# Optimization experiments

Hardware: AMD Instinct MI355X
Metric: run time of the kernel (lower is better)

Reference implementation:

```python
import jax, jax.numpy as jnp
import numpy as np

L, K, H = 8000, 48, 128
SCALE = 30.0
LN_EPS = 1e-5


def _gelu(x):
    return jax.nn.gelu(x, approximate=False)


def _ln(x, s, o):
    mu = x.mean(-1, keepdims=True)
    var = ((x - mu) ** 2).mean(-1, keepdims=True)
    return (x - mu) * jax.lax.rsqrt(var + LN_EPS) * s + o


def setup_inputs() -> dict:
    key = jax.random.key(0)
    ks = jax.random.split(key, 24)

    def w(k, fan_in, fan_out):
        return (jax.random.normal(k, (fan_in, fan_out), jnp.float32) / np.sqrt(fan_in)).astype(jnp.float32)

    inp = {
        "h_V": jax.random.normal(ks[0], (L, H), jnp.float32),
        "h_E": jax.random.normal(ks[1], (L, K, H), jnp.float32),
        "E_idx": jax.random.randint(ks[2], (L, K), 0, L, jnp.int32),
        "mask_V": jnp.ones((L,), jnp.float32),
        "mask_attend": jnp.ones((L, K), jnp.float32),
        # node-message MLP (W1 consumes [h_V, h_E, gathered h_V] = 3H)
        "W1_w": w(ks[3], 3 * H, H), "W1_b": jnp.zeros((H,), jnp.float32),
        "W2_w": w(ks[4], H, H),     "W2_b": jnp.zeros((H,), jnp.float32),
        "W3_w": w(ks[5], H, H),     "W3_b": jnp.zeros((H,), jnp.float32),
        # edge-update MLP
        "W11_w": w(ks[6], 3 * H, H), "W11_b": jnp.zeros((H,), jnp.float32),
        "W12_w": w(ks[7], H, H),     "W12_b": jnp.zeros((H,), jnp.float32),
        "W13_w": w(ks[8], H, H),     "W13_b": jnp.zeros((H,), jnp.float32),
        # position-wise FFN (H -> 4H -> H)
        "Wi_w": w(ks[9], H, 4 * H),  "Wi_b": jnp.zeros((4 * H,), jnp.float32),
        "Wo_w": w(ks[10], 4 * H, H), "Wo_b": jnp.zeros((H,), jnp.float32),
        # layer norms
        "n1_s": jnp.ones((H,), jnp.float32), "n1_o": jnp.zeros((H,), jnp.float32),
        "n2_s": jnp.ones((H,), jnp.float32), "n2_o": jnp.zeros((H,), jnp.float32),
        "n3_s": jnp.ones((H,), jnp.float32), "n3_o": jnp.zeros((H,), jnp.float32),
    }
    return inp


def _forward(h_V, h_E, mask_V, mask_attend, E_idx,
             W1_w, W1_b, W2_w, W2_b, W3_w, W3_b,
             W11_w, W11_b, W12_w, W12_b, W13_w, W13_b,
             Wi_w, Wi_b, Wo_w, Wo_b,
             n1_s, n1_o, n2_s, n2_o, n3_s, n3_o):
    # --- node update ---
    nb = h_V[E_idx]                                          # (L,K,H) gather_nodes
    hv_exp = jnp.broadcast_to(h_V[:, None, :], nb.shape)     # (L,K,H)
    h_EV = jnp.concatenate([hv_exp, h_E, nb], -1)            # (L,K,3H)
    m = _gelu(h_EV @ W1_w + W1_b)
    m = _gelu(m @ W2_w + W2_b)
    m = m @ W3_w + W3_b                                      # (L,K,H)
    m = mask_attend[..., None] * m
    dh = m.sum(-2) / SCALE                                   # (L,H)
    hV = _ln(h_V + dh, n1_s, n1_o)                           # dropout = identity (eval)
    d = _gelu(hV @ Wi_w + Wi_b) @ Wo_w + Wo_b                # FFN
    hV = _ln(hV + d, n2_s, n2_o)
    hV = mask_V[:, None] * hV
    # --- edge update ---
    nb2 = hV[E_idx]                                          # (L,K,H)
    hv_exp2 = jnp.broadcast_to(hV[:, None, :], nb2.shape)
    h_EV2 = jnp.concatenate([hv_exp2, h_E, nb2], -1)         # (L,K,3H)
    m2 = _gelu(h_EV2 @ W11_w + W11_b)
    m2 = _gelu(m2 @ W12_w + W12_b)
    m2 = m2 @ W13_w + W13_b
    hE = _ln(h_E + m2, n3_s, n3_o)
    return hV, hE


def reference(h_V, h_E, E_idx, mask_V, mask_attend,
              W1_w, W1_b, W2_w, W2_b, W3_w, W3_b,
              W11_w, W11_b, W12_w, W12_b, W13_w, W13_b,
              Wi_w, Wi_b, Wo_w, Wo_b,
              n1_s, n1_o, n2_s, n2_o, n3_s, n3_o):
    return _forward(h_V, h_E, mask_V, mask_attend, E_idx,
                    W1_w, W1_b, W2_w, W2_b, W3_w, W3_b,
                    W11_w, W11_b, W12_w, W12_b, W13_w, W13_b,
                    Wi_w, Wi_b, Wo_w, Wo_b,
                    n1_s, n1_o, n2_s, n2_o, n3_s, n3_o)
```

## Files before the change

### kernel.cpp

```cpp
#include <hip/hip_runtime.h>
#include <cstddef>
#include <cstdint>
#include <cmath>

#define LDIM 8000
#define KNB  48
#define HDIM 128

typedef short  bf16x8 __attribute__((ext_vector_type(8)));
typedef float  f32x4  __attribute__((ext_vector_type(4)));

__device__ __forceinline__ float gelu_f(float x) {
    return 0.5f * x * (1.0f + erff(x * 0.70710678118654752440f));
}
__device__ __forceinline__ unsigned short bf16_rne(float x) {
    unsigned u = __float_as_uint(x);
    return (unsigned short)((u + 0x7FFFu + ((u >> 16) & 1u)) >> 16);
}
__device__ __forceinline__ float bf16_f(unsigned short h) {
    return __uint_as_float((unsigned)h << 16);
}
__device__ __forceinline__ void split2(float x, short& h, short& l) {
    unsigned short hb = bf16_rne(x);
    h = (short)hb;
    l = (short)bf16_rne(x - bf16_f(hb));
}
__device__ __forceinline__ void mm3(f32x4& c, bf16x8 ah, bf16x8 al, bf16x8 bh, bf16x8 bl) {
    c = __builtin_amdgcn_mfma_f32_16x16x32_bf16(ah, bh, c, 0, 0, 0);
    c = __builtin_amdgcn_mfma_f32_16x16x32_bf16(ah, bl, c, 0, 0, 0);
    c = __builtin_amdgcn_mfma_f32_16x16x32_bf16(al, bh, c, 0, 0, 0);
}

__global__ void wsplit_kernel(const float* __restrict__ W, short* __restrict__ dst, int K) {
    int t = blockIdx.x * 256 + threadIdx.x;
    if (t >= K * 128) return;
    int k = t >> 7, n = t & 127;
    float x = W[t];
    short h, l; split2(x, h, l);
    dst[(size_t)n * K + k]         = h;
    dst[(size_t)(128 + n) * K + k] = l;
}

template<bool EDGE>
__global__ __launch_bounds__(256, 2)
void msg_mfma_kernel(const float* __restrict__ hv_src,
                     const float* __restrict__ hEin,
                     const int*   __restrict__ Eidx,
                     const float* __restrict__ mask_att,
                     const short* __restrict__ WaT,
                     const short* __restrict__ WbT,
                     const short* __restrict__ WcT,
                     const float* __restrict__ ba,
                     const float* __restrict__ bb,
                     const float* __restrict__ bc,
                     const float* __restrict__ ln_s,
                     const float* __restrict__ ln_o,
                     float* __restrict__ outp)
{
    __shared__ union {
        short xc[2][96][40];
        short cp[2][96][136];
        float xb[96 * 132];
    } sm;
    __shared__ float mask_s[96];

    const int bid  = blockIdx.x;
    const int n0   = bid * 2;
    const int tid  = threadIdx.x;
    const int w    = tid >> 6;
    const int lane = tid & 63;
    const int lr   = lane & 15;
    const int hgr  = lane >> 4;
    const int colA = w * 32 + lr;
    const int colB = colA + 16;

    if constexpr (!EDGE) {
        if (tid < 96) mask_s[tid] = mask_att[(size_t)n0 * KNB + tid];
    }

    int trow[3], tq[3];
    const float* pV[3]; const float* pE[3]; const float* pN[3];
#pragma unroll
    for (int it = 0; it < 3; it++) {
        const int t   = tid + it * 256;
        const int row = t >> 3, q = t & 7;
        trow[it] = row; tq[it] = q;
        const int node = n0 + (row >= 48 ? 1 : 0);
        pV[it] = hv_src + (size_t)node * HDIM + q * 4;
        pE[it] = hEin + ((size_t)n0 * KNB + row) * HDIM + q * 4;
        const int nb = Eidx[n0 * KNB + row];
        pN[it] = hv_src + (size_t)nb * HDIM + q * 4;
    }

    f32x4 acc[12];

    {
        const float bA = ba[colA], bB = ba[colB];
#pragma unroll
        for (int mt = 0; mt < 6; mt++) {
            acc[mt*2+0] = (f32x4){bA, bA, bA, bA};
            acc[mt*2+1] = (f32x4){bB, bB, bB, bB};
        }
    }
    {
        const short* WaL = WaT + 128 * 384;
#pragma unroll 1
        for (int ks = 0; ks < 12; ks++) {
            const int ko = ks * 32 + hgr * 8;
            bf16x8 bh0 = *(const bf16x8*)(WaT + (size_t)colA * 384 + ko);
            bf16x8 bl0 = *(const bf16x8*)(WaL + (size_t)colA * 384 + ko);
            bf16x8 bh1 = *(const bf16x8*)(WaT + (size_t)colB * 384 + ko);
            bf16x8 bl1 = *(const bf16x8*)(WaL + (size_t)colB * 384 + ko);
            __syncthreads();
            {
                const int seg = ks >> 2, co = (ks & 3) * 32;
#pragma unroll
                for (int it = 0; it < 3; it++) {
                    const float* p = (seg == 0) ? pV[it] : (seg == 1) ? pE[it] : pN[it];
                    const float4 v = *(const float4*)(p + co);
                    short h0,l0,h1,l1,h2,l2,h3,l3;
                    split2(v.x,h0,l0); split2(v.y,h1,l1);
                    split2(v.z,h2,l2); split2(v.w,h3,l3);
                    *(short4*)&sm.xc[0][trow[it]][tq[it]*4] = make_short4(h0,h1,h2,h3);
                    *(short4*)&sm.xc[1][trow[it]][tq[it]*4] = make_short4(l0,l1,l2,l3);
                }
            }
            __syncthreads();
#pragma unroll
            for (int mt = 0; mt < 6; mt++) {
                bf16x8 ah = *(const bf16x8*)&sm.xc[0][mt*16 + lr][hgr*8];
                bf16x8 al = *(const bf16x8*)&sm.xc[1][mt*16 + lr][hgr*8];
                mm3(acc[mt*2+0], ah, al, bh0, bl0);
                mm3(acc[mt*2+1], ah, al, bh1, bl1);
            }
        }
    }
    __syncthreads();
#pragma unroll
    for (int mt = 0; mt < 6; mt++)
#pragma unroll
    for (int nt = 0; nt < 2; nt++) {
        const int col = w*32 + nt*16 + lr;
        const f32x4 a = acc[mt*2+nt];
#pragma unroll
        for (int j = 0; j < 4; j++) {
            const int row = mt*16 + hgr*4 + j;
            short h, l; split2(gelu_f(a[j]), h, l);
            sm.cp[0][row][col] = h;
            sm.cp[1][row][col] = l;
        }
    }
    __syncthreads();

    {
        const short* WbL = WbT + 128 * 128;
        const float bA = bb[colA], bB = bb[colB];
#pragma unroll
        for (int mt = 0; mt < 6; mt++) {
            acc[mt*2+0] = (f32x4){bA, bA, bA, bA};
            acc[mt*2+1] = (f32x4){bB, bB, bB, bB};
        }
#pragma unroll 1
        for (int ks = 0; ks < 4; ks++) {
            const int ko = ks * 32 + hgr * 8;
            bf16x8 bh0 = *(const bf16x8*)(WbT + (size_t)colA * 128 + ko);
            bf16x8 bl0 = *(const bf16x8*)(WbL + (size_t)colA * 128 + ko);
            bf16x8 bh1 = *(const bf16x8*)(WbT + (size_t)colB * 128 + ko);
            bf16x8 bl1 = *(const bf16x8*)(WbL + (size_t)colB * 128 + ko);
#pragma unroll
            for (int mt = 0; mt < 6; mt++) {
                bf16x8 ah = *(const bf16x8*)&sm.cp[0][mt*16 + lr][ko];
                bf16x8 al = *(const bf16x8*)&sm.cp[1][mt*16 + lr][ko];
                mm3(acc[mt*2+0], ah, al, bh0, bl0);
                mm3(acc[mt*2+1], ah, al, bh1, bl1);
            }
        }
        __syncthreads();
#pragma unroll
        for (int mt = 0; mt < 6; mt++)
#pragma unroll
        for (int nt = 0; nt < 2; nt++) {
            const int col = w*32 + nt*16 + lr;
            const f32x4 a = acc[mt*2+nt];
#pragma unroll
            for (int j = 0; j < 4; j++) {
                const int row = mt*16 + hgr*4 + j;
                short h, l; split2(gelu_f(a[j]), h, l);
                sm.cp[0][row][col] = h;
                sm.cp[1][row][col] = l;
            }
        }
        __syncthreads();
    }

    {
        const short* WcL = WcT + 128 * 128;
        const float bA = bc[colA], bB = bc[colB];
#pragma unroll
        for (int mt = 0; mt < 6; mt++) {
            acc[mt*2+0] = (f32x4){bA, bA, bA, bA};
            acc[mt*2+1] = (f32x4){bB, bB, bB, bB};
        }
#pragma unroll 1
        for (int ks = 0; ks < 4; ks++) {
            const int ko = ks * 32 + hgr * 8;
            bf16x8 bh0 = *(const bf16x8*)(WcT + (size_t)colA * 128 + ko);
            bf16x8 bl0 = *(const bf16x8*)(WcL + (size_t)colA * 128 + ko);
            bf16x8 bh1 = *(const bf16x8*)(WcT + (size_t)colB * 128 + ko);
            bf16x8 bl1 = *(const bf16x8*)(WcL + (size_t)colB * 128 + ko);
#pragma unroll
            for (int mt = 0; mt < 6; mt++) {
                bf16x8 ah = *(const bf16x8*)&sm.cp[0][mt*16 + lr][ko];
                bf16x8 al = *(const bf16x8*)&sm.cp[1][mt*16 + lr][ko];
                mm3(acc[mt*2+0], ah, al, bh0, bl0);
                mm3(acc[mt*2+1], ah, al, bh1, bl1);
            }
        }
        __syncthreads();
    }

    if constexpr (!EDGE) {
        float s[4] = {0.f, 0.f, 0.f, 0.f};
#pragma unroll
        for (int mt = 0; mt < 6; mt++) {
            const int nodei = (mt >= 3) ? 1 : 0;
#pragma unroll
            for (int j = 0; j < 4; j++) {
                const float m = mask_s[mt*16 + hgr*4 + j];
                s[nodei*2+0] = fmaf(m, acc[mt*2+0][j], s[nodei*2+0]);
                s[nodei*2+1] = fmaf(m, acc[mt*2+1][j], s[nodei*2+1]);
            }
        }
#pragma unroll
        for (int i = 0; i < 4; i++) {
            s[i] += __shfl_xor(s[i], 16, 64);
            s[i] += __shfl_xor(s[i], 32, 64);
        }
        if (lane < 16) {
            outp[(size_t)n0 * HDIM + colA]       = s[0] * (1.0f / 30.0f);
            outp[(size_t)n0 * HDIM + colB]       = s[1] * (1.0f / 30.0f);
            outp[(size_t)(n0+1) * HDIM + colA]   = s[2] * (1.0f / 30.0f);
            outp[(size_t)(n0+1) * HDIM + colB]   = s[3] * (1.0f / 30.0f);
        }
    } else {
#pragma unroll
        for (int mt = 0; mt < 6; mt++)
#pragma unroll
        for (int nt = 0; nt < 2; nt++) {
            const int col = w*32 + nt*16 + lr;
            const f32x4 a = acc[mt*2+nt];
#pragma unroll
            for (int j = 0; j < 4; j++) {
                const int row = mt*16 + hgr*4 + j;
                const float he = hEin[((size_t)n0 * KNB + row) * HDIM + col];
                sm.xb[row * 132 + col] = a[j] + he;
            }
        }
        __syncthreads();
        for (int r = w; r < 96; r += 4) {
            const float x0 = sm.xb[r * 132 + lane];
            const float x1 = sm.xb[r * 132 + 64 + lane];
            float su = x0 + x1;
#pragma unroll
            for (int off = 32; off; off >>= 1) su += __shfl_xor(su, off, 64);
            const float mu = su * (1.0f / 128.0f);
            const float d0 = x0 - mu, d1 = x1 - mu;
            float v = d0 * d0 + d1 * d1;
#pragma unroll
            for (int off = 32; off; off >>= 1) v += __shfl_xor(v, off, 64);
            const float rs = rsqrtf(v * (1.0f / 128.0f) + 1e-5f);
            const size_t base = ((size_t)n0 * KNB + r) * HDIM;
            outp[base + lane]      = d0 * rs * ln_s[lane]      + ln_o[lane];
            outp[base + 64 + lane] = d1 * rs * ln_s[64 + lane] + ln_o[64 + lane];
        }
    }
}

template<int RT, int KDIM>
__device__ __forceinline__ void gemm_block(
    const float* __restrict__ A, const int lda,
    const float* __restrict__ Wg, const int wstride,
    float* __restrict__ Wst,
    float acc[RT][4], const int rg, const int jg, const int tid)
{
#pragma unroll 1
    for (int ci = 0; ci < KDIM / 32; ci++) {
        __syncthreads();
#pragma unroll
        for (int e = tid; e < 1024; e += 256) {
            const int i  = e >> 5;
            const int j4 = (e & 31) << 2;
            *(float4*)(Wst + i * 128 + j4) =
                *(const float4*)(Wg + (size_t)(ci * 32 + i) * wstride + j4);
        }
        __syncthreads();
#pragma unroll
        for (int ii = 0; ii < 32; ii += 4) {
            float4 xr[RT];
#pragma unroll
            for (int rr = 0; rr < RT; rr++)
                xr[rr] = *(const float4*)(A + (rg * RT + rr) * lda + ci * 32 + ii);
#pragma unroll
            for (int q = 0; q < 4; q++) {
                const float4 wv = *(const float4*)(Wst + (ii + q) * 128 + (jg << 2));
#pragma unroll
                for (int rr = 0; rr < RT; rr++) {
                    const float x = (q == 0) ? xr[rr].x : (q == 1) ? xr[rr].y
                                  : (q == 2) ? xr[rr].z : xr[rr].w;
                    acc[rr][0] = fmaf(x, wv.x, acc[rr][0]);
                    acc[rr][1] = fmaf(x, wv.y, acc[rr][1]);
                    acc[rr][2] = fmaf(x, wv.z, acc[rr][2]);
                    acc[rr][3] = fmaf(x, wv.w, acc[rr][3]);
                }
            }
        }
    }
}

template<int NPART>
__global__ __launch_bounds__(256, 2)
void node_update_kernel(const float* __restrict__ hV,
                        const float* __restrict__ dhp,
                        const float* __restrict__ maskV,
                        const float* __restrict__ Wi, const float* __restrict__ bi,
                        const float* __restrict__ Wo, const float* __restrict__ bo,
                        const float* __restrict__ n1s, const float* __restrict__ n1o,
                        const float* __restrict__ n2s, const float* __restrict__ n2o,
                        float* __restrict__ outp)
{
    __shared__ float hv1[32 * 128];
    __shared__ float Wst[32 * 128];
    __shared__ float tb[32 * 128];

    const int l0  = blockIdx.x * 32;
    const int tid = threadIdx.x;
    const int w = tid >> 6, ln = tid & 63;

    for (int r = w; r < 32; r += 4) {
        const int l = l0 + r;
        const size_t b = (size_t)l * 128;
        float x0 = hV[b + ln], x1 = hV[b + 64 + ln];
#pragma unroll
        for (int p = 0; p < NPART; p++) {
            x0 += dhp[((size_t)l * NPART + p) * 128 + ln];
            x1 += dhp[((size_t)l * NPART + p) * 128 + 64 + ln];
        }
        float s = x0 + x1;
#pragma unroll
        for (int off = 32; off; off >>= 1) s += __shfl_xor(s, off, 64);
        const float mu = s * (1.0f / 128.0f);
        const float d0 = x0 - mu, d1 = x1 - mu;
        float v = d0 * d0 + d1 * d1;
#pragma unroll
        for (int off = 32; off; off >>= 1) v += __shfl_xor(v, off, 64);
        const float rs = rsqrtf(v * (1.0f / 128.0f) + 1e-5f);
        hv1[r * 128 + ln]      = d0 * rs * n1s[ln]      + n1o[ln];
        hv1[r * 128 + 64 + ln] = d1 * rs * n1s[64 + ln] + n1o[64 + ln];
    }

    const int rg = tid >> 5, jg = tid & 31;
    float dacc[4][4];
#pragma unroll
    for (int rr = 0; rr < 4; rr++)
#pragma unroll
        for (int q = 0; q < 4; q++) dacc[rr][q] = bo[(jg << 2) + q];

#pragma unroll 1
    for (int hc = 0; hc < 4; hc++) {
        float tacc[4][4];
#pragma unroll
        for (int rr = 0; rr < 4; rr++)
#pragma unroll
            for (int q = 0; q < 4; q++) tacc[rr][q] = bi[hc * 128 + (jg << 2) + q];
        gemm_block<4, 128>(hv1, 128, Wi + hc * 128, 512, Wst, tacc, rg, jg, tid);
        __syncthreads();
#pragma unroll
        for (int rr = 0; rr < 4; rr++)
#pragma unroll
            for (int q = 0; q < 4; q++)
                tb[(rg * 4 + rr) * 128 + (jg << 2) + q] = gelu_f(tacc[rr][q]);
        gemm_block<4, 128>(tb, 128, Wo + (size_t)hc * 128 * 128, 128, Wst, dacc, rg, jg, tid);
    }
    __syncthreads();
#pragma unroll
    for (int rr = 0; rr < 4; rr++)
#pragma unroll
        for (int q = 0; q < 4; q++)
            tb[(rg * 4 + rr) * 128 + (jg << 2) + q] = dacc[rr][q];
    __syncthreads();

    for (int r = w; r < 32; r += 4) {
        const int l = l0 + r;
        const float x0 = hv1[r * 128 + ln]      + tb[r * 128 + ln];
        const float x1 = hv1[r * 128 + 64 + ln] + tb[r * 128 + 64 + ln];
        float s = x0 + x1;
#pragma unroll
        for (int off = 32; off; off >>= 1) s += __shfl_xor(s, off, 64);
        const float mu = s * (1.0f / 128.0f);
        const float d0 = x0 - mu, d1 = x1 - mu;
        float v = d0 * d0 + d1 * d1;
#pragma unroll
        for (int off = 32; off; off >>= 1) v += __shfl_xor(v, off, 64);
        const float rs = rsqrtf(v * (1.0f / 128.0f) + 1e-5f);
        const float mv = maskV[l];
        outp[(size_t)l * 128 + ln]      = mv * (d0 * rs * n2s[ln]      + n2o[ln]);
        outp[(size_t)l * 128 + 64 + ln] = mv * (d1 * rs * n2s[64 + ln] + n2o[64 + ln]);
    }
}

template<bool EDGE>
__global__ __launch_bounds__(256, 2)
void msg_kernel(const float* __restrict__ hv_src,
                const float* __restrict__ hEin,
                const int*   __restrict__ Eidx,
                const float* __restrict__ mask_att,
                const float* __restrict__ Wa, const float* __restrict__ ba,
                const float* __restrict__ Wb, const float* __restrict__ bb,
                const float* __restrict__ Wc3, const float* __restrict__ bc,
                const float* __restrict__ ln_s, const float* __restrict__ ln_o,
                float* __restrict__ outp)
{
    __shared__ float xs[24 * 384];
    __shared__ float Wst[32 * 128];
    __shared__ float Cb[24 * 128];

    const int bid = blockIdx.x;
    const int l   = bid >> 1;
    const int k0  = (bid & 1) * 24;
    const int tid = threadIdx.x;

#pragma unroll
    for (int e = tid; e < 24 * 32; e += 256) {
        const int r  = e >> 5;
        const int c4 = (e & 31) << 2;
        const int k  = k0 + r;
        const int nidx = Eidx[l * KNB + k];
        const float4 hv4 = *(const float4*)(hv_src + (size_t)l * HDIM + c4);
        const float4 he4 = *(const float4*)(hEin + ((size_t)l * KNB + k) * HDIM + c4);
        const float4 nb4 = *(const float4*)(hv_src + (size_t)nidx * HDIM + c4);
        *(float4*)(xs + r * 384 +       c4) = hv4;
        *(float4*)(xs + r * 384 + 128 + c4) = he4;
        *(float4*)(xs + r * 384 + 256 + c4) = nb4;
    }

    const int rg = tid >> 5;
    const int jg = tid & 31;
    float acc[3][4];

#pragma unroll
    for (int rr = 0; rr < 3; rr++)
#pragma unroll
        for (int q = 0; q < 4; q++) acc[rr][q] = ba[(jg << 2) + q];
    gemm_block<3, 384>(xs, 384, Wa, 128, Wst, acc, rg, jg, tid);
    __syncthreads();
#pragma unroll
    for (int rr = 0; rr < 3; rr++)
#pragma unroll
        for (int q = 0; q < 4; q++)
            Cb[(rg * 3 + rr) * 128 + (jg << 2) + q] = gelu_f(acc[rr][q]);

#pragma unroll
    for (int rr = 0; rr < 3; rr++)
#pragma unroll
        for (int q = 0; q < 4; q++) acc[rr][q] = bb[(jg << 2) + q];
    gemm_block<3, 128>(Cb, 128, Wb, 128, Wst, acc, rg, jg, tid);
    __syncthreads();
#pragma unroll
    for (int rr = 0; rr < 3; rr++)
#pragma unroll
        for (int q = 0; q < 4; q++)
            Cb[(rg * 3 + rr) * 128 + (jg << 2) + q] = gelu_f(acc[rr][q]);

#pragma unroll
    for (int rr = 0; rr < 3; rr++)
#pragma unroll
        for (int q = 0; q < 4; q++) acc[rr][q] = bc[(jg << 2) + q];
    gemm_block<3, 128>(Cb, 128, Wc3, 128, Wst, acc, rg, jg, tid);
    __syncthreads();

    if constexpr (!EDGE) {
        float psum[4] = {0.f, 0.f, 0.f, 0.f};
#pragma unroll
        for (int rr = 0; rr < 3; rr++) {
            const int k = k0 + rg * 3 + rr;
            const float mval = mask_att[l * KNB + k];
#pragma unroll
            for (int q = 0; q < 4; q++) psum[q] = fmaf(mval, acc[rr][q], psum[q]);
        }
#pragma unroll
        for (int q = 0; q < 4; q++) Cb[rg * 128 + (jg << 2) + q] = psum[q];
        __syncthreads();
        if (tid < 128) {
            float s = 0.f;
#pragma unroll
            for (int g = 0; g < 8; g++) s += Cb[g * 128 + tid];
            outp[(size_t)bid * 128 + tid] = s * (1.0f / 30.0f);
        }
    } else {
#pragma unroll
        for (int rr = 0; rr < 3; rr++)
#pragma unroll
            for (int q = 0; q < 4; q++)
                Cb[(rg * 3 + rr) * 128 + (jg << 2) + q] = acc[rr][q];
        __syncthreads();
        const int w = tid >> 6, ln = tid & 63;
        for (int r = w; r < 24; r += 4) {
            const float x0 = Cb[r * 128 + ln]      + xs[r * 384 + 128 + ln];
            const float x1 = Cb[r * 128 + 64 + ln] + xs[r * 384 + 192 + ln];
            float s = x0 + x1;
#pragma unroll
            for (int off = 32; off; off >>= 1) s += __shfl_xor(s, off, 64);
            const float mu = s * (1.0f / 128.0f);
            const float d0 = x0 - mu, d1 = x1 - mu;
            float v = d0 * d0 + d1 * d1;
#pragma unroll
            for (int off = 32; off; off >>= 1) v += __shfl_xor(v, off, 64);
            const float rs = rsqrtf(v * (1.0f / 128.0f) + 1e-5f);
            const size_t base = ((size_t)(l * KNB + k0 + r)) * 128;
            outp[base + ln]      = d0 * rs * ln_s[ln]      + ln_o[ln];
            outp[base + 64 + ln] = d1 * rs * ln_s[64 + ln] + ln_o[64 + ln];
        }
    }
}

extern "C" void kernel_launch(void* const* d_in, const int* in_sizes, int n_in,
                              void* d_out, int out_size, void* d_ws, size_t ws_size,
                              hipStream_t stream) {
    const float* hV      = (const float*)d_in[0];
    const float* hE      = (const float*)d_in[1];
    const int*   Eidx    = (const int*)  d_in[2];
    const float* maskV   = (const float*)d_in[3];
    const float* maskAtt = (const float*)d_in[4];
    const float* W1  = (const float*)d_in[5];  const float* b1  = (const float*)d_in[6];
    const float* W2  = (const float*)d_in[7];  const float* b2  = (const float*)d_in[8];
    const float* W3  = (const float*)d_in[9];  const float* b3  = (const float*)d_in[10];
    const float* W11 = (const float*)d_in[11]; const float* b11 = (const float*)d_in[12];
    const float* W12 = (const float*)d_in[13]; const float* b12 = (const float*)d_in[14];
    const float* W13 = (const float*)d_in[15]; const float* b13 = (const float*)d_in[16];
    const float* Wi  = (const float*)d_in[17]; const float* bi  = (const float*)d_in[18];
    const float* Wo  = (const float*)d_in[19]; const float* bo  = (const float*)d_in[20];
    const float* n1s = (const float*)d_in[21]; const float* n1o = (const float*)d_in[22];
    const float* n2s = (const float*)d_in[23]; const float* n2o = (const float*)d_in[24];
    const float* n3s = (const float*)d_in[25]; const float* n3o = (const float*)d_in[26];

    float* outF  = (float*)d_out;
    float* hVout = outF;
    float* hEout = outF + (size_t)LDIM * HDIM;

    const size_t O_W1T  = 0;
    const size_t O_W2T  = 196608;
    const size_t O_W3T  = 262144;
    const size_t O_W11T = 327680;
    const size_t O_W12T = 524288;
    const size_t O_W13T = 589824;
    const size_t O_DH   = 655360;
    const size_t WS_NEED = O_DH + (size_t)LDIM * HDIM * sizeof(float);

    if (ws_size >= WS_NEED) {
        char* wsb = (char*)d_ws;
        short* W1T  = (short*)(wsb + O_W1T);
        short* W2T  = (short*)(wsb + O_W2T);
        short* W3T  = (short*)(wsb + O_W3T);
        short* W11T = (short*)(wsb + O_W11T);
        short* W12T = (short*)(wsb + O_W12T);
        short* W13T = (short*)(wsb + O_W13T);
        float* dh   = (float*)(wsb + O_DH);

        wsplit_kernel<<<192, 256, 0, stream>>>(W1,  W1T,  384);
        wsplit_kernel<<< 64, 256, 0, stream>>>(W2,  W2T,  128);
        wsplit_kernel<<< 64, 256, 0, stream>>>(W3,  W3T,  128);
        wsplit_kernel<<<192, 256, 0, stream>>>(W11, W11T, 384);
        wsplit_kernel<<< 64, 256, 0, stream>>>(W12, W12T, 128);
        wsplit_kernel<<< 64, 256, 0, stream>>>(W13, W13T, 128);

        msg_mfma_kernel<false><<<LDIM / 2, 256, 0, stream>>>(
            hV, hE, Eidx, maskAtt, W1T, W2T, W3T, b1, b2, b3, nullptr, nullptr, dh);

        node_update_kernel<1><<<LDIM / 32, 256, 0, stream>>>(
            hV, dh, maskV, Wi, bi, Wo, bo, n1s, n1o, n2s, n2o, hVout);

        msg_mfma_kernel<true><<<LDIM / 2, 256, 0, stream>>>(
            hVout, hE, Eidx, nullptr, W11T, W12T, W13T, b11, b12, b13, n3s, n3o, hEout);
    } else {
        const size_t dh_bytes = (size_t)LDIM * 2 * HDIM * sizeof(float);
        float* dhp = (ws_size >= dh_bytes) ? (float*)d_ws : hEout;

        msg_kernel<false><<<LDIM * 2, 256, 0, stream>>>(
            hV, hE, Eidx, maskAtt, W1, b1, W2, b2, W3, b3, nullptr, nullptr, dhp);

        node_update_kernel<2><<<LDIM / 32, 256, 0, stream>>>(
            hV, dhp, maskV, Wi, bi, Wo, bo, n1s, n1o, n2s, n2o, hVout);

        msg_kernel<true><<<LDIM * 2, 256, 0, stream>>>(
            hVout, hE, Eidx, nullptr, W11, b11, W12, b12, W13, b13, n3s, n3o, hEout);
    }
}
```

Before: 1.299 ms.

## Presplit node features to bf16 hi/lo, double-buffer GEMM staging, swizzle LDS rows

Adds a kernel that splits the node-feature matrix into bf16 hi/lo planes once, so the message kernel gathers pre-split halves instead of converting gathered fp32 values per tile. The first GEMM's input staging is double-buffered in shared memory with register prefetch of the next tile and its weights, which removes one barrier per k-step. The 128-wide GEMMs also prefetch weights, and a row permutation is applied when storing activations to cut LDS bank conflicts. The node-update kernel now uses 16-node blocks for more parallelism. The cost is two extra split passes and extra workspace memory.

```diff
diff --git a/kernel.cpp b/kernel.cpp
--- a/kernel.cpp
+++ b/kernel.cpp
@@ -35,18 +35,25 @@
     int t = blockIdx.x * 256 + threadIdx.x;
     if (t >= K * 128) return;
     int k = t >> 7, n = t & 127;
-    float x = W[t];
-    short h, l; split2(x, h, l);
+    short h, l; split2(W[t], h, l);
     dst[(size_t)n * K + k]         = h;
     dst[(size_t)(128 + n) * K + k] = l;
 }
 
+__global__ void hvsplit_kernel(const float* __restrict__ src, short* __restrict__ dst) {
+    int t = blockIdx.x * 256 + threadIdx.x;
+    if (t >= LDIM * HDIM) return;
+    short h, l; split2(src[t], h, l);
+    dst[t] = h;
+    dst[LDIM * HDIM + t] = l;
+}
+
 template<bool EDGE>
 __global__ __launch_bounds__(256, 2)
-void msg_mfma_kernel(const float* __restrict__ hv_src,
-                     const float* __restrict__ hEin,
+void msg_mfma_kernel(const float* __restrict__ hEin,
                      const int*   __restrict__ Eidx,
                      const float* __restrict__ mask_att,
+                     const short* __restrict__ hvP,
                      const short* __restrict__ WaT,
                      const short* __restrict__ WbT,
                      const short* __restrict__ WcT,
@@ -58,7 +65,7 @@
                      float* __restrict__ outp)
 {
     __shared__ union {
-        short xc[2][96][40];
+        short xc[2][2][96][40];
         short cp[2][96][136];
         float xb[96 * 132];
     } sm;
@@ -71,153 +78,152 @@
     const int lane = tid & 63;
     const int lr   = lane & 15;
     const int hgr  = lane >> 4;
+    const int plr  = ((lr & 2) << 2) | ((2 * (lr >> 2) + (lr & 1) + 2 * (lr & 2)) & 7);
     const int colA = w * 32 + lr;
     const int colB = colA + 16;
+    const int PL   = LDIM * HDIM;
 
     if constexpr (!EDGE) {
         if (tid < 96) mask_s[tid] = mask_att[(size_t)n0 * KNB + tid];
     }
 
-    int trow[3], tq[3];
-    const float* pV[3]; const float* pE[3]; const float* pN[3];
+    int xoff[3];
+    int hvo[3], nbo[3];
+    const float* pE[3];
 #pragma unroll
     for (int it = 0; it < 3; it++) {
-        const int t   = tid + it * 256;
-        const int row = t >> 3, q = t & 7;
-        trow[it] = row; tq[it] = q;
+        const int t = tid + it * 256, row = t >> 3, q = t & 7;
+        xoff[it] = row * 40 + q * 4;
         const int node = n0 + (row >= 48 ? 1 : 0);
-        pV[it] = hv_src + (size_t)node * HDIM + q * 4;
-        pE[it] = hEin + ((size_t)n0 * KNB + row) * HDIM + q * 4;
-        const int nb = Eidx[n0 * KNB + row];
-        pN[it] = hv_src + (size_t)nb * HDIM + q * 4;
+        hvo[it] = node * HDIM + q * 4;
+        nbo[it] = Eidx[n0 * KNB + row] * HDIM + q * 4;
+        pE[it]  = hEin + ((size_t)n0 * KNB + row) * HDIM + q * 4;
     }
 
     f32x4 acc[12];
 
-    {
-        const float bA = ba[colA], bB = ba[colB];
+    uint4 sr[3];
+    auto LOADR = [&](int ks) {
+#pragma unroll
+        for (int it = 0; it < 3; it++) {
+            const int seg = ks >> 2, co = (ks & 3) * 32;
+            if (seg == 1) {
+                sr[it] = *(const uint4*)(pE[it] + co);
+            } else {
+                const int base = (seg == 0 ? hvo[it] : nbo[it]) + co;
+                const uint2 h = *(const uint2*)(hvP + base);
+                const uint2 l = *(const uint2*)(hvP + PL + base);
+                sr[it] = make_uint4(h.x, h.y, l.x, l.y);
+            }
+        }
+    };
+    auto WRITES = [&](int ks, int b) {
+        short* p0 = &sm.xc[b][0][0][0];
+        short* p1 = &sm.xc[b][1][0][0];
+#pragma unroll
+        for (int it = 0; it < 3; it++) {
+            if ((ks >> 2) == 1) {
+                const float4 v = *(const float4*)&sr[it];
+                short h0,l0,h1,l1,h2,l2,h3,l3;
+                split2(v.x,h0,l0); split2(v.y,h1,l1);
+                split2(v.z,h2,l2); split2(v.w,h3,l3);
+                *(short4*)(p0 + xoff[it]) = make_short4(h0,h1,h2,h3);
+                *(short4*)(p1 + xoff[it]) = make_short4(l0,l1,l2,l3);
+            } else {
+                *(uint2*)(p0 + xoff[it]) = make_uint2(sr[it].x, sr[it].y);
+                *(uint2*)(p1 + xoff[it]) = make_uint2(sr[it].z, sr[it].w);
+            }
+        }
+    };
+    auto BLOAD = [&](const short* Th, int stride, int ks,
+                     bf16x8& b0, bf16x8& b1, bf16x8& b2, bf16x8& b3) {
+        const short* Tl = Th + 128 * stride;
+        const int ko = ks * 32 + hgr * 8;
+        b0 = *(const bf16x8*)(Th + (size_t)colA * stride + ko);
+        b1 = *(const bf16x8*)(Tl + (size_t)colA * stride + ko);
+        b2 = *(const bf16x8*)(Th + (size_t)colB * stride + ko);
+        b3 = *(const bf16x8*)(Tl + (size_t)colB * stride + ko);
+    };
+    auto storeC = [&]() {
+#pragma unroll
+        for (int mt = 0; mt < 6; mt++)
+#pragma unroll
+        for (int nt = 0; nt < 2; nt++) {
+            const int col = w * 32 + nt * 16 + lr;
+            const f32x4 a = acc[mt * 2 + nt];
+#pragma unroll
+            for (int j = 0; j < 4; j++) {
+                const int prw = mt * 16 +
+                    (((j >> 1) << 3) | ((2 * hgr + (j & 1) + 4 * (j >> 1)) & 7));
+                short h, l; split2(gelu_f(a[j]), h, l);
+                sm.cp[0][prw][col] = h;
+                sm.cp[1][prw][col] = l;
+            }
+        }
+    };
+    auto gemmK128 = [&](const short* T, const float* bias) {
+        const float bA = bias[colA], bB = bias[colB];
 #pragma unroll
         for (int mt = 0; mt < 6; mt++) {
             acc[mt*2+0] = (f32x4){bA, bA, bA, bA};
             acc[mt*2+1] = (f32x4){bB, bB, bB, bB};
         }
-    }
+        bf16x8 c0,c1,c2,c3,d0,d1,d2,d3;
+        BLOAD(T, 128, 0, c0,c1,c2,c3);
+#pragma unroll 1
+        for (int ks = 0; ks < 4; ks++) {
+            if (ks < 3) BLOAD(T, 128, ks + 1, d0,d1,d2,d3);
+            const int ko = ks * 32 + hgr * 8;
+#pragma unroll
+            for (int mt = 0; mt < 6; mt++) {
+                bf16x8 ah = *(const bf16x8*)&sm.cp[0][mt*16 + plr][ko];
+                bf16x8 al = *(const bf16x8*)&sm.cp[1][mt*16 + plr][ko];
+                mm3(acc[mt*2+0], ah, al, c0, c1);
+                mm3(acc[mt*2+1], ah, al, c2, c3);
+            }
+            c0=d0; c1=d1; c2=d2; c3=d3;
+        }
+    };
+
     {
-        const short* WaL = WaT + 128 * 384;
-#pragma unroll 1
-        for (int ks = 0; ks < 12; ks++) {
-            const int ko = ks * 32 + hgr * 8;
-            bf16x8 bh0 = *(const bf16x8*)(WaT + (size_t)colA * 384 + ko);
-            bf16x8 bl0 = *(const bf16x8*)(WaL + (size_t)colA * 384 + ko);
-            bf16x8 bh1 = *(const bf16x8*)(WaT + (size_t)colB * 384 + ko);
-            bf16x8 bl1 = *(const bf16x8*)(WaL + (size_t)colB * 384 + ko);
-            __syncthreads();
-            {
-                const int seg = ks >> 2, co = (ks & 3) * 32;
-#pragma unroll
-                for (int it = 0; it < 3; it++) {
-                    const float* p = (seg == 0) ? pV[it] : (seg == 1) ? pE[it] : pN[it];
-                    const float4 v = *(const float4*)(p + co);
-                    short h0,l0,h1,l1,h2,l2,h3,l3;
-                    split2(v.x,h0,l0); split2(v.y,h1,l1);
-                    split2(v.z,h2,l2); split2(v.w,h3,l3);
-                    *(short4*)&sm.xc[0][trow[it]][tq[it]*4] = make_short4(h0,h1,h2,h3);
-                    *(short4*)&sm.xc[1][trow[it]][tq[it]*4] = make_short4(l0,l1,l2,l3);
-                }
-            }
-            __syncthreads();
-#pragma unroll
-            for (int mt = 0; mt < 6; mt++) {
-                bf16x8 ah = *(const bf16x8*)&sm.xc[0][mt*16 + lr][hgr*8];
-                bf16x8 al = *(const bf16x8*)&sm.xc[1][mt*16 + lr][hgr*8];
-                mm3(acc[mt*2+0], ah, al, bh0, bl0);
-                mm3(acc[mt*2+1], ah, al, bh1, bl1);
-            }
-        }
-    }
-    __syncthreads();
-#pragma unroll
-    for (int mt = 0; mt < 6; mt++)
-#pragma unroll
-    for (int nt = 0; nt < 2; nt++) {
-        const int col = w*32 + nt*16 + lr;
-        const f32x4 a = acc[mt*2+nt];
-#pragma unroll
-        for (int j = 0; j < 4; j++) {
-            const int row = mt*16 + hgr*4 + j;
-            short h, l; split2(gelu_f(a[j]), h, l);
-            sm.cp[0][row][col] = h;
-            sm.cp[1][row][col] = l;
-        }
-    }
-    __syncthreads();
-
-    {
-        const short* WbL = WbT + 128 * 128;
-        const float bA = bb[colA], bB = bb[colB];
+        const float bA = ba[colA], bB = ba[colB];
 #pragma unroll
         for (int mt = 0; mt < 6; mt++) {
             acc[mt*2+0] = (f32x4){bA, bA, bA, bA};
             acc[mt*2+1] = (f32x4){bB, bB, bB, bB};
         }
+    }
+    {
+        bf16x8 c0,c1,c2,c3,d0,d1,d2,d3;
+        LOADR(0);
+        BLOAD(WaT, 384, 0, c0,c1,c2,c3);
+        WRITES(0, 0);
+        __syncthreads();
 #pragma unroll 1
-        for (int ks = 0; ks < 4; ks++) {
-            const int ko = ks * 32 + hgr * 8;
-            bf16x8 bh0 = *(const bf16x8*)(WbT + (size_t)colA * 128 + ko);
-            bf16x8 bl0 = *(const bf16x8*)(WbL + (size_t)colA * 128 + ko);
-            bf16x8 bh1 = *(const bf16x8*)(WbT + (size_t)colB * 128 + ko);
-            bf16x8 bl1 = *(const bf16x8*)(WbL + (size_t)colB * 128 + ko);
+        for (int ks = 0; ks < 12; ks++) {
+            if (ks < 11) { LOADR(ks + 1); BLOAD(WaT, 384, ks + 1, d0,d1,d2,d3); }
+            const int b = ks & 1;
 #pragma unroll
             for (int mt = 0; mt < 6; mt++) {
-                bf16x8 ah = *(const bf16x8*)&sm.cp[0][mt*16 + lr][ko];
-                bf16x8 al = *(const bf16x8*)&sm.cp[1][mt*16 + lr][ko];
-                mm3(acc[mt*2+0], ah, al, bh0, bl0);
-                mm3(acc[mt*2+1], ah, al, bh1, bl1);
-            }
-        }
-        __syncthreads();
-#pragma unroll
-        for (int mt = 0; mt < 6; mt++)
-#pragma unroll
-        for (int nt = 0; nt < 2; nt++) {
-            const int col = w*32 + nt*16 + lr;
-            const f32x4 a = acc[mt*2+nt];
-#pragma unroll
-            for (int j = 0; j < 4; j++) {
-                const int row = mt*16 + hgr*4 + j;
-                short h, l; split2(gelu_f(a[j]), h, l);
-                sm.cp[0][row][col] = h;
-                sm.cp[1][row][col] = l;
-            }
-        }
-        __syncthreads();
-    }
-
-    {
-        const short* WcL = WcT + 128 * 128;
-        const float bA = bc[colA], bB = bc[colB];
-#pragma unroll
-        for (int mt = 0; mt < 6; mt++) {
-            acc[mt*2+0] = (f32x4){bA, bA, bA, bA};
-            acc[mt*2+1] = (f32x4){bB, bB, bB, bB};
-        }
-#pragma unroll 1
-        for (int ks = 0; ks < 4; ks++) {
-            const int ko = ks * 32 + hgr * 8;
-            bf16x8 bh0 = *(const bf16x8*)(WcT + (size_t)colA * 128 + ko);
-            bf16x8 bl0 = *(const bf16x8*)(WcL + (size_t)colA * 128 + ko);
-            bf16x8 bh1 = *(const bf16x8*)(WcT + (size_t)colB * 128 + ko);
-            bf16x8 bl1 = *(const bf16x8*)(WcL + (size_t)colB * 128 + ko);
-#pragma unroll
-            for (int mt = 0; mt < 6; mt++) {
-                bf16x8 ah = *(const bf16x8*)&sm.cp[0][mt*16 + lr][ko];
-                bf16x8 al = *(const bf16x8*)&sm.cp[1][mt*16 + lr][ko];
-                mm3(acc[mt*2+0], ah, al, bh0, bl0);
-                mm3(acc[mt*2+1], ah, al, bh1, bl1);
-            }
-        }
-        __syncthreads();
-    }
+                bf16x8 ah = *(const bf16x8*)&sm.xc[b][0][mt*16 + lr][hgr*8];
+                bf16x8 al = *(const bf16x8*)&sm.xc[b][1][mt*16 + lr][hgr*8];
+                mm3(acc[mt*2+0], ah, al, c0, c1);
+                mm3(acc[mt*2+1], ah, al, c2, c3);
+            }
+            if (ks < 11) WRITES(ks + 1, b ^ 1);
+            __syncthreads();
+            c0=d0; c1=d1; c2=d2; c3=d3;
+        }
+    }
+    storeC();
+    __syncthreads();
+
+    gemmK128(WbT, bb);
+    __syncthreads();
+    storeC();
+    __syncthreads();
+
+    gemmK128(WcT, bc);
 
     if constexpr (!EDGE) {
         float s[4] = {0.f, 0.f, 0.f, 0.f};
@@ -237,12 +243,13 @@
             s[i] += __shfl_xor(s[i], 32, 64);
         }
         if (lane < 16) {
-            outp[(size_t)n0 * HDIM + colA]       = s[0] * (1.0f / 30.0f);
-            outp[(size_t)n0 * HDIM + colB]       = s[1] * (1.0f / 30.0f);
-            outp[(size_t)(n0+1) * HDIM + colA]   = s[2] * (1.0f / 30.0f);
-            outp[(size_t)(n0+1) * HDIM + colB]   = s[3] * (1.0f / 30.0f);
+            outp[(size_t)n0 * HDIM + colA]     = s[0] * (1.0f / 30.0f);
+            outp[(size_t)n0 * HDIM + colB]     = s[1] * (1.0f / 30.0f);
+            outp[(size_t)(n0+1) * HDIM + colA] = s[2] * (1.0f / 30.0f);
+            outp[(size_t)(n0+1) * HDIM + colB] = s[3] * (1.0f / 30.0f);
         }
     } else {
+        __syncthreads();
 #pragma unroll
         for (int mt = 0; mt < 6; mt++)
 #pragma unroll
@@ -317,7 +324,7 @@
     }
 }
 
-template<int NPART>
+template<int NODES, int RT, int NPART>
 __global__ __launch_bounds__(256, 2)
 void node_update_kernel(const float* __restrict__ hV,
                         const float* __restrict__ dhp,
@@ -328,15 +335,15 @@
                         const float* __restrict__ n2s, const float* __restrict__ n2o,
                         float* __restrict__ outp)
 {
-    __shared__ float hv1[32 * 128];
+    __shared__ float hv1[NODES * 128];
     __shared__ float Wst[32 * 128];
-    __shared__ float tb[32 * 128];
-
-    const int l0  = blockIdx.x * 32;
+    __shared__ float tb[NODES * 128];
+
+    const int l0  = blockIdx.x * NODES;
     const int tid = threadIdx.x;
     const int w = tid >> 6, ln = tid & 63;
 
-    for (int r = w; r < 32; r += 4) {
+    for (int r = w; r < NODES; r += 4) {
         const int l = l0 + r;
         const size_t b = (size_t)l * 128;
         float x0 = hV[b + ln], x1 = hV[b + 64 + ln];
@@ -359,37 +366,37 @@
     }
 
     const int rg = tid >> 5, jg = tid & 31;
-    float dacc[4][4];
-#pragma unroll
-    for (int rr = 0; rr < 4; rr++)
+    float dacc[RT][4];
+#pragma unroll
+    for (int rr = 0; rr < RT; rr++)
 #pragma unroll
         for (int q = 0; q < 4; q++) dacc[rr][q] = bo[(jg << 2) + q];
 
 #pragma unroll 1
     for (int hc = 0; hc < 4; hc++) {
-        float tacc[4][4];
-#pragma unroll
-        for (int rr = 0; rr < 4; rr++)
+        float tacc[RT][4];
+#pragma unroll
+        for (int rr = 0; rr < RT; rr++)
 #pragma unroll
             for (int q = 0; q < 4; q++) tacc[rr][q] = bi[hc * 128 + (jg << 2) + q];
-        gemm_block<4, 128>(hv1, 128, Wi + hc * 128, 512, Wst, tacc, rg, jg, tid);
-        __syncthreads();
-#pragma unroll
-        for (int rr = 0; rr < 4; rr++)
+        gemm_block<RT, 128>(hv1, 128, Wi + hc * 128, 512, Wst, tacc, rg, jg, tid);
+        __syncthreads();
+#pragma unroll
+        for (int rr = 0; rr < RT; rr++)
 #pragma unroll
             for (int q = 0; q < 4; q++)
-                tb[(rg * 4 + rr) * 128 + (jg << 2) + q] = gelu_f(tacc[rr][q]);
-        gemm_block<4, 128>(tb, 128, Wo + (size_t)hc * 128 * 128, 128, Wst, dacc, rg, jg, tid);
-    }
-    __syncthreads();
-#pragma unroll
-    for (int rr = 0; rr < 4; rr++)
+                tb[(rg * RT + rr) * 128 + (jg << 2) + q] = gelu_f(tacc[rr][q]);
+        gemm_block<RT, 128>(tb, 128, Wo + (size_t)hc * 128 * 128, 128, Wst, dacc, rg, jg, tid);
+    }
+    __syncthreads();
+#pragma unroll
+    for (int rr = 0; rr < RT; rr++)
 #pragma unroll
         for (int q = 0; q < 4; q++)
-            tb[(rg * 4 + rr) * 128 + (jg << 2) + q] = dacc[rr][q];
-    __syncthreads();
-
-    for (int r = w; r < 32; r += 4) {
+            tb[(rg * RT + rr) * 128 + (jg << 2) + q] = dacc[rr][q];
+    __syncthreads();
+
+    for (int r = w; r < NODES; r += 4) {
         const int l = l0 + r;
         const float x0 = hv1[r * 128 + ln]      + tb[r * 128 + ln];
         const float x1 = hv1[r * 128 + 64 + ln] + tb[r * 128 + 64 + ln];
@@ -554,7 +561,8 @@
     const size_t O_W12T = 524288;
     const size_t O_W13T = 589824;
     const size_t O_DH   = 655360;
-    const size_t WS_NEED = O_DH + (size_t)LDIM * HDIM * sizeof(float);
+    const size_t O_HVP  = O_DH + (size_t)LDIM*HDIM*4;
+    const size_t WS_NEED = O_HVP + (size_t)2*LDIM*HDIM*2;
 
     if (ws_size >= WS_NEED) {
         char* wsb = (char*)d_ws;
@@ -565,6 +573,7 @@
         short* W12T = (short*)(wsb + O_W12T);
         short* W13T = (short*)(wsb + O_W13T);
         float* dh   = (float*)(wsb + O_DH);
+        short* hvP  = (short*)(wsb + O_HVP);
 
         wsplit_kernel<<<192, 256, 0, stream>>>(W1,  W1T,  384);
         wsplit_kernel<<< 64, 256, 0, stream>>>(W2,  W2T,  128);
@@ -572,15 +581,18 @@
         wsplit_kernel<<<192, 256, 0, stream>>>(W11, W11T, 384);
         wsplit_kernel<<< 64, 256, 0, stream>>>(W12, W12T, 128);
         wsplit_kernel<<< 64, 256, 0, stream>>>(W13, W13T, 128);
+        hvsplit_kernel<<<(LDIM*HDIM + 255)/256, 256, 0, stream>>>(hV, hvP);
 
         msg_mfma_kernel<false><<<LDIM / 2, 256, 0, stream>>>(
-            hV, hE, Eidx, maskAtt, W1T, W2T, W3T, b1, b2, b3, nullptr, nullptr, dh);
-
-        node_update_kernel<1><<<LDIM / 32, 256, 0, stream>>>(
+            hE, Eidx, maskAtt, hvP, W1T, W2T, W3T, b1, b2, b3, nullptr, nullptr, dh);
+
+        node_update_kernel<16, 2, 1><<<LDIM / 16, 256, 0, stream>>>(
             hV, dh, maskV, Wi, bi, Wo, bo, n1s, n1o, n2s, n2o, hVout);
 
+        hvsplit_kernel<<<(LDIM*HDIM + 255)/256, 256, 0, stream>>>(hVout, hvP);
+
         msg_mfma_kernel<true><<<LDIM / 2, 256, 0, stream>>>(
-            hVout, hE, Eidx, nullptr, W11T, W12T, W13T, b11, b12, b13, n3s, n3o, hEout);
+            hE, Eidx, nullptr, hvP, W11T, W12T, W13T, b11, b12, b13, n3s, n3o, hEout);
     } else {
         const size_t dh_bytes = (size_t)LDIM * 2 * HDIM * sizeof(float);
         float* dhp = (ws_size >= dh_bytes) ? (float*)d_ws : hEout;
@@ -588,7 +600,7 @@
         msg_kernel<false><<<LDIM * 2, 256, 0, stream>>>(
             hV, hE, Eidx, maskAtt, W1, b1, W2, b2, W3, b3, nullptr, nullptr, dhp);
 
-        node_update_kernel<2><<<LDIM / 32, 256, 0, stream>>>(
+        node_update_kernel<32, 4, 2><<<LDIM / 32, 256, 0, stream>>>(
             hV, dhp, maskV, Wi, bi, Wo, bo, n1s, n1o, n2s, n2o, hVout);
 
         msg_kernel<true><<<LDIM * 2, 256, 0, stream>>>(
```

New measurement: 1.164 ms. -10.3%, faster.
